# Optimization experiments

Hardware: AMD Instinct MI355X
Metric: run time of the kernel (lower is better)

## Reference

```python
import jax, jax.numpy as jnp
import numpy as np

NEG_SLOPE = 0.2  # leaky_relu_negative_slope


def setup_inputs() -> dict:
    key = jax.random.key(0)
    k = jax.random.split(key, 6)
    N = 1024          # n_nodes == nei_nodes (forced by the asserts in forward)
    IN = 256          # in_features
    OUT = 256         # out_features (nei_embedding feature dim, since linear_r = Linear(out_features, ...))
    H, F = 4, 64      # n_heads, n_hidden = out_features // n_heads
    h = jax.random.normal(k[0], (N, IN), dtype=jnp.float32)
    nei_embedding = jax.random.normal(k[1], (N, OUT), dtype=jnp.float32)
    adj_mat = jax.random.randint(k[2], (N, N), 0, 2).astype(jnp.float32)
    scale = 0.05
    w_l = jax.random.normal(k[3], (IN, H * F), dtype=jnp.float32) * scale   # linear_l.weight.T
    w_r = jax.random.normal(k[4], (OUT, H * F), dtype=jnp.float32) * scale  # linear_r.weight.T
    attn_w = jax.random.normal(k[5], (F,), dtype=jnp.float32) * scale       # attn.weight (1, F) -> (F,)
    return {"h": h, "nei_embedding": nei_embedding, "adj_mat": adj_mat,
            "w_l": w_l, "w_r": w_r, "attn_w": attn_w, "use_elu": 1}


def reference(h, nei_embedding, adj_mat, w_l, w_r, attn_w, use_elu):
    N = h.shape[0]
    M = nei_embedding.shape[0]
    F = attn_w.shape[0]
    H = w_l.shape[1] // F
    g_l = (h @ w_l).reshape(N, H, F)              # (N, H, F)
    g_r = (nei_embedding @ w_r).reshape(M, H, F)  # (M, H, F)
    # Torch does repeat/repeat_interleave then view(n, m, H, F); with the
    # assert-enforced n == m this is exactly g_sum[i, j] = g_l[j] + g_r[i].
    g_sum = g_r[:, None, :, :] + g_l[None, :, :, :]          # (N, N, H, F)
    e = jnp.einsum("nmhf,f->nmh", jax.nn.leaky_relu(g_sum, NEG_SLOPE), attn_w)
    adj_t = adj_mat.T[:, :, None]                             # (M, N, 1) -> broadcasts over heads
    e = jnp.where(adj_t == 0, -jnp.inf, e)
    exp_attention = jnp.exp(e)
    weighted = exp_attention * adj_t                          # (N, N, H)
    denom = jnp.sum(weighted, axis=1, keepdims=True)
    a = weighted / denom                                      # masked softmax over neighbors
    # dropout is identity at inference
    attn_res = jnp.einsum("ijh,jhf->ihf", a, g_r)            # (N, H, F)
    if use_elu:
        attn_res = jax.nn.elu(attn_res)
    return attn_res.reshape(N, H * F)  # is_concat=True
```

## Files before the change

kernel.cpp:

```cpp
#include <hip/hip_runtime.h>
#include <math.h>

#define NN 1024
#define KK 256
#define NH 4
#define FD 64
#define HF 256
#define RL 68
#define NG 17

typedef __attribute__((ext_vector_type(16))) float fx16;
typedef __attribute__((ext_vector_type(4)))  float fx4;

#define OFF_GR    0
#define OFF_GL2   262144
#define OFF_GR2   540672
#define OFF_CL    819200
#define OFF_CR    823296
#define OFF_DENP  827392
#define OFF_P     1089536
#define OFF_ACCP  5283840
#define OFF_DEST  13672448
#define OFF_ABSW  13672512
#define OFF_GPOS  13672576

__global__ void gatv2_prep(const float* __restrict__ aw, float* __restrict__ ws)
{
    const int f = threadIdx.x;
    const float wv = aw[f];
    const bool pos = (wv >= 0.f);
    const unsigned long long mask = __ballot(pos);
    const int npos  = __popcll(mask);
    const int npos4 = (npos + 3) & ~3;
    const unsigned long long lt = (1ull << f) - 1ull;
    const int prank = __popcll(mask & lt);
    const int nrank = __popcll(~mask & lt);
    const int dest  = pos ? prank : (npos4 + nrank);
    ((int*)(ws + OFF_DEST))[f] = dest;
    (ws + OFF_ABSW)[f] = fabsf(wv);
    if (f == 0) ((int*)(ws + OFF_GPOS))[0] = npos4 >> 2;
}

__global__ __launch_bounds__(256) void gatv2_gemm(
    const float* __restrict__ hmat, const float* __restrict__ nei,
    const float* __restrict__ w_l, const float* __restrict__ w_r,
    const float* __restrict__ aw, float* __restrict__ ws)
{
    __shared__ float sA[16*260];
    const int t   = threadIdx.x;
    const int mb  = blockIdx.x;
    const int hd  = blockIdx.y;
    const int mat = blockIdx.z;
    const float* A = mat ? nei : hmat;
    const float* W = mat ? w_r : w_l;
    float* CC = ws + (mat ? OFF_CR : OFF_CL);

    #pragma unroll
    for (int rep = 0; rep < 4; ++rep) {
        const int flat = rep*256 + t;
        const int r = flat >> 6, c = (flat & 63) << 2;
        *(float4*)&sA[r*260 + c] = *(const float4*)&A[(size_t)(mb*16 + r)*KK + c];
    }
    __syncthreads();

    const int m  = t >> 4;
    const int nq = t & 15;
    const int ng = hd*64 + (nq << 2);
    const float* Wp = W + ng;

    float4 acc = make_float4(0.f, 0.f, 0.f, 0.f);
    #pragma unroll 4
    for (int k0 = 0; k0 < KK; k0 += 4) {
        const float4 a4 = *(const float4*)&sA[m*260 + k0];
        const float4 w0 = *(const float4*)(Wp + (size_t)(k0+0)*HF);
        const float4 w1 = *(const float4*)(Wp + (size_t)(k0+1)*HF);
        const float4 w2 = *(const float4*)(Wp + (size_t)(k0+2)*HF);
        const float4 w3 = *(const float4*)(Wp + (size_t)(k0+3)*HF);
        acc.x += a4.x*w0.x; acc.y += a4.x*w0.y; acc.z += a4.x*w0.z; acc.w += a4.x*w0.w;
        acc.x += a4.y*w1.x; acc.y += a4.y*w1.y; acc.z += a4.y*w1.z; acc.w += a4.y*w1.w;
        acc.x += a4.z*w2.x; acc.y += a4.z*w2.y; acc.z += a4.z*w2.z; acc.w += a4.z*w2.w;
        acc.x += a4.w*w3.x; acc.y += a4.w*w3.y; acc.z += a4.w*w3.z; acc.w += a4.w*w3.w;
    }

    const int node = mb*16 + m;
    if (mat) *(float4*)&(ws + OFF_GR)[(size_t)node*HF + ng] = acc;

    {
        const int*   destp = (const int*)(ws + OFF_DEST);
        const int4   dv = ((const int4*)destp)[nq];
        const float4 av = ((const float4*)(ws + OFF_ABSW))[nq];
        float* g2 = ws + (mat ? OFF_GR2 : OFF_GL2) + ((size_t)node*NH + hd)*RL;
        g2[dv.x] = av.x*acc.x; g2[dv.y] = av.y*acc.y;
        g2[dv.z] = av.z*acc.z; g2[dv.w] = av.w*acc.w;
    }

    {
        const float4 w4 = ((const float4*)aw)[nq];
        float wd = w4.x*acc.x + w4.y*acc.y + w4.z*acc.z + w4.w*acc.w;
        wd += __shfl_xor(wd, 1);
        wd += __shfl_xor(wd, 2);
        wd += __shfl_xor(wd, 4);
        wd += __shfl_xor(wd, 8);
        if (nq == 0) CC[hd*NN + node] = 0.6f*wd;
    }
}

__global__ __launch_bounds__(256, 2) void gatv2_e(
    const float* __restrict__ wsro, const float* __restrict__ adj,
    float* __restrict__ P, float* __restrict__ denP)
{
    __shared__ float sgl[16*RL];
    __shared__ float scl[16];
    const float* gl2 = wsro + OFF_GL2;
    const float* gr2 = wsro + OFF_GR2;
    const float* cl  = wsro + OFF_CL;
    const float* cr  = wsro + OFF_CR;
    const int t  = threadIdx.x;
    const int jc = blockIdx.x;
    const int ib = blockIdx.y;
    const int hh = blockIdx.z;
    const int i0 = ib*512 + t;
    const int i1 = i0 + 256;
    const int j0 = jc*16;

    for (int idx = t; idx < 16*NG; idx += 256) {
        const int r = idx / NG, c = idx - r*NG;
        *(float4*)&sgl[r*RL + (c<<2)] =
            *(const float4*)&gl2[((size_t)(j0+r)*NH + hh)*RL + (c<<2)];
    }
    if (t < 16) scl[t] = cl[hh*NN + j0 + t];

    fx4 ga[NG], gb[NG];
    {
        const fx4* pa = (const fx4*)(gr2 + ((size_t)i0*NH + hh)*RL);
        const fx4* pb = (const fx4*)(gr2 + ((size_t)i1*NH + hh)*RL);
        #pragma unroll
        for (int g = 0; g < NG; ++g) { ga[g] = pa[g]; gb[g] = pb[g]; }
    }
    #pragma unroll
    for (int g = 0; g < NG; ++g) { asm volatile("" : "+v"(ga[g])); }
    #pragma unroll
    for (int g = 0; g < NG; ++g) { asm volatile("" : "+v"(gb[g])); }

    const int gpos = ((const int*)(wsro + OFF_GPOS))[0];
    float mg[NG];
    #pragma unroll
    for (int g = 0; g < NG; ++g) mg[g] = (g < gpos) ? 0.4f : -0.4f;
    #pragma unroll
    for (int g = 0; g < NG; ++g) { asm volatile("" : "+v"(mg[g])); }

    const float cr0 = cr[hh*NN + i0];
    const float cr1 = cr[hh*NN + i1];

    float den0 = 0.f, den1 = 0.f;
    __syncthreads();

    #pragma unroll 2
    for (int jj = 0; jj < 16; ++jj) {
        const int j = j0 + jj;
        const float mk0 = adj[(size_t)j*NN + i0];
        const float mk1 = adj[(size_t)j*NN + i1];
        float a0 = 0.f, a1 = 0.f;
        #pragma unroll
        for (int g = 0; g < NG; ++g) {
            const fx4 b  = *(const fx4*)&sgl[jj*RL + (g<<2)];
            const fx4 va = b + ga[g];
            const fx4 vb = b + gb[g];
            const float sa = (fabsf(va[0]) + fabsf(va[1])) + (fabsf(va[2]) + fabsf(va[3]));
            const float sb = (fabsf(vb[0]) + fabsf(vb[1])) + (fabsf(vb[2]) + fabsf(vb[3]));
            a0 = fmaf(mg[g], sa, a0);
            a1 = fmaf(mg[g], sb, a1);
        }
        const float clj = scl[jj];
        const float p0 = (mk0 != 0.f) ? __expf(cr0 + clj + a0) : 0.f;
        const float p1 = (mk1 != 0.f) ? __expf(cr1 + clj + a1) : 0.f;
        den0 += p0; den1 += p1;
        const size_t pb = ((size_t)hh*NN + j)*NN;
        P[pb + i0] = p0;
        P[pb + i1] = p1;
    }
    denP[((size_t)jc*NH + hh)*NN + i0] = den0;
    denP[((size_t)jc*NH + hh)*NN + i1] = den1;
}

#define PVFMA(G0, G1, PP)                                           \
    { _Pragma("unroll") for (int q = 0; q < 4; ++q) {               \
        acc[q].x   += (PP)*G0[q*4+0]; acc[q].y   += (PP)*G0[q*4+1]; \
        acc[q].z   += (PP)*G0[q*4+2]; acc[q].w   += (PP)*G0[q*4+3]; \
        acc[4+q].x += (PP)*G1[q*4+0]; acc[4+q].y += (PP)*G1[q*4+1]; \
        acc[4+q].z += (PP)*G1[q*4+2]; acc[4+q].w += (PP)*G1[q*4+3]; } }

__global__ __launch_bounds__(256, 4) void gatv2_pv(
    const float* __restrict__ wsro, float* __restrict__ accP)
{
    __shared__ float sT[256*36];
    const float* g_r = wsro + OFF_GR;
    const float* P   = wsro + OFF_P;
    const int t  = threadIdx.x;
    const int jc = blockIdx.x;
    const int ib = blockIdx.y;
    const int fs = blockIdx.z;
    const int hh = fs >> 1;
    const int f0 = hh*64 + (fs & 1)*32;
    const int i  = ib*256 + t;

    float4 acc[8];
    #pragma unroll
    for (int q = 0; q < 8; ++q) acc[q] = make_float4(0.f,0.f,0.f,0.f);

    const int j0 = jc*32;
    const size_t pb0 = ((size_t)hh*NN)*NN + i;

    fx16 a0, a1, b0, b1;
    {
        const float* gp = g_r + (size_t)j0*HF + f0;
        asm volatile(
            "s_load_dwordx16 %0, %2, 0x0\n\t"
            "s_load_dwordx16 %1, %2, 0x40\n\t"
            "s_waitcnt lgkmcnt(0)"
            : "=s"(a0), "=s"(a1) : "s"(gp));
    }
    float pA = P[pb0 + (size_t)j0*NN];

    for (int jj = 0; jj < 32; jj += 2) {
        const int j = j0 + jj;
        {
            const float* gp = g_r + (size_t)(j+1)*HF + f0;
            asm volatile(
                "s_load_dwordx16 %0, %2, 0x0\n\t"
                "s_load_dwordx16 %1, %2, 0x40"
                : "=s"(b0), "=s"(b1) : "s"(gp));
        }
        const float pB = P[pb0 + (size_t)(j+1)*NN];
        PVFMA(a0, a1, pA)
        asm volatile("s_waitcnt lgkmcnt(0)");
        {
            const int j2 = (jj + 2 < 32) ? (j + 2) : j0;
            const float* gp = g_r + (size_t)j2*HF + f0;
            asm volatile(
                "s_load_dwordx16 %0, %2, 0x0\n\t"
                "s_load_dwordx16 %1, %2, 0x40"
                : "=s"(a0), "=s"(a1) : "s"(gp));
            pA = P[pb0 + (size_t)j2*NN];
        }
        PVFMA(b0, b1, pB)
        asm volatile("s_waitcnt lgkmcnt(0)");
    }

    #pragma unroll
    for (int q = 0; q < 4; ++q) {
        *(float4*)&sT[t*36 + q*4] = acc[q];
        *(float4*)&sT[t*36 + 16 + q*4] = acc[4+q];
    }
    __syncthreads();
    #pragma unroll
    for (int rep = 0; rep < 8; ++rep) {
        const int idx = rep*256 + t;
        const int il = idx >> 3, fq = idx & 7;
        const float4 v = *(const float4*)&sT[il*36 + fq*4];
        *(float4*)&accP[(size_t)jc*(NN*HF) + (size_t)(ib*256 + il)*HF + f0 + fq*4] = v;
    }
}

__global__ __launch_bounds__(256) void gatv2_fin(
    const float* __restrict__ accP, const float* __restrict__ denP,
    const int* __restrict__ use_elu, float* __restrict__ out)
{
    const int idx4 = blockIdx.x*256 + threadIdx.x;
    const int i  = idx4 >> 6;
    const int hh = (idx4 >> 4) & 3;
    float4 s = make_float4(0.f,0.f,0.f,0.f);
    for (int c = 0; c < 32; ++c) {
        const float4 v = *(const float4*)&accP[(size_t)c*(NN*HF) + (size_t)idx4*4];
        s.x += v.x; s.y += v.y; s.z += v.z; s.w += v.w;
    }
    float d = 0.f;
    for (int c = 0; c < 64; ++c) d += denP[((size_t)c*NH + hh)*NN + i];
    const float rd = 1.f / d;
    float4 r = make_float4(s.x*rd, s.y*rd, s.z*rd, s.w*rd);
    if (*use_elu != 0) {
        r.x = (r.x > 0.f) ? r.x : expm1f(r.x);
        r.y = (r.y > 0.f) ? r.y : expm1f(r.y);
        r.z = (r.z > 0.f) ? r.z : expm1f(r.z);
        r.w = (r.w > 0.f) ? r.w : expm1f(r.w);
    }
    ((float4*)out)[idx4] = r;
}

extern "C" void kernel_launch(void* const* d_in, const int* in_sizes, int n_in,
                              void* d_out, int out_size, void* d_ws, size_t ws_size,
                              hipStream_t stream)
{
    const float* hmat = (const float*)d_in[0];
    const float* nei  = (const float*)d_in[1];
    const float* adj  = (const float*)d_in[2];
    const float* w_l  = (const float*)d_in[3];
    const float* w_r  = (const float*)d_in[4];
    const float* aw   = (const float*)d_in[5];
    const int*   uel  = (const int*)d_in[6];
    float* out = (float*)d_out;
    float* ws  = (float*)d_ws;

    hipMemsetAsync((void*)(ws + OFF_GL2), 0, (size_t)2*278528*sizeof(float), stream);
    hipLaunchKernelGGL(gatv2_prep, dim3(1), dim3(64), 0, stream, aw, ws);
    hipLaunchKernelGGL(gatv2_gemm, dim3(64,4,2), dim3(256), 0, stream,
                       hmat, nei, w_l, w_r, aw, ws);
    hipLaunchKernelGGL(gatv2_e, dim3(64,2,4), dim3(256), 0, stream,
                       ws, adj, ws + OFF_P, ws + OFF_DENP);
    hipLaunchKernelGGL(gatv2_pv, dim3(32,4,8), dim3(256), 0, stream,
                       ws, ws + OFF_ACCP);
    hipLaunchKernelGGL(gatv2_fin, dim3((NN*HF)/1024), dim3(256), 0, stream,
                       ws + OFF_ACCP, ws + OFF_DENP, uel, out);
}
```

Baseline: 147.2 us.

## Load g_l rows via scalar loads instead of LDS, one node per thread

The attention-score kernel stops staging the 16 g_l rows and cl values in shared memory. Each iteration now loads the wave-uniform g_l row and cl value straight into scalar registers with inline s_load_dwordx16 instructions, so the vector ALU reads them as SGPR operands. Each thread now handles one node instead of two, the grid doubles in y, and launch bounds rise to three blocks per SM for more occupancy. The cost is a full lgkmcnt wait on every j iteration, which serializes scalar memory latency, and half the reuse of each loaded g_l row.

```diff
diff --git a/kernel.cpp b/kernel.cpp
--- a/kernel.cpp
+++ b/kernel.cpp
@@ -105,12 +105,21 @@
     }
 }
 
-__global__ __launch_bounds__(256, 2) void gatv2_e(
+#define EGRP(RS, QB, q)                                             \
+    { const fx4 gq = g[(QB)+(q)];                                   \
+      const float t0 = RS[(q)*4+0] + gq[0];                         \
+      const float t1 = RS[(q)*4+1] + gq[1];                         \
+      const float t2 = RS[(q)*4+2] + gq[2];                         \
+      const float t3 = RS[(q)*4+3] + gq[3];                         \
+      a = fmaf(mg[(QB)+(q)],                                        \
+               (fabsf(t0)+fabsf(t1))+(fabsf(t2)+fabsf(t3)), a); }
+
+#define EBLK4(RS, QB) EGRP(RS, QB, 0) EGRP(RS, QB, 1) EGRP(RS, QB, 2) EGRP(RS, QB, 3)
+
+__global__ __launch_bounds__(256, 3) void gatv2_e(
     const float* __restrict__ wsro, const float* __restrict__ adj,
     float* __restrict__ P, float* __restrict__ denP)
 {
-    __shared__ float sgl[16*RL];
-    __shared__ float scl[16];
     const float* gl2 = wsro + OFF_GL2;
     const float* gr2 = wsro + OFF_GR2;
     const float* cl  = wsro + OFF_CL;
@@ -119,68 +128,56 @@
     const int jc = blockIdx.x;
     const int ib = blockIdx.y;
     const int hh = blockIdx.z;
-    const int i0 = ib*512 + t;
-    const int i1 = i0 + 256;
+    const int i  = ib*256 + t;
     const int j0 = jc*16;
 
-    for (int idx = t; idx < 16*NG; idx += 256) {
-        const int r = idx / NG, c = idx - r*NG;
-        *(float4*)&sgl[r*RL + (c<<2)] =
-            *(const float4*)&gl2[((size_t)(j0+r)*NH + hh)*RL + (c<<2)];
-    }
-    if (t < 16) scl[t] = cl[hh*NN + j0 + t];
-
-    fx4 ga[NG], gb[NG];
+    fx4 g[NG];
     {
-        const fx4* pa = (const fx4*)(gr2 + ((size_t)i0*NH + hh)*RL);
-        const fx4* pb = (const fx4*)(gr2 + ((size_t)i1*NH + hh)*RL);
+        const fx4* gp = (const fx4*)(gr2 + ((size_t)i*NH + hh)*RL);
         #pragma unroll
-        for (int g = 0; g < NG; ++g) { ga[g] = pa[g]; gb[g] = pb[g]; }
-    }
-    #pragma unroll
-    for (int g = 0; g < NG; ++g) { asm volatile("" : "+v"(ga[g])); }
-    #pragma unroll
-    for (int g = 0; g < NG; ++g) { asm volatile("" : "+v"(gb[g])); }
+        for (int q = 0; q < NG; ++q) g[q] = gp[q];
+    }
+    #pragma unroll
+    for (int q = 0; q < NG; ++q) { asm volatile("" : "+v"(g[q])); }
 
     const int gpos = ((const int*)(wsro + OFF_GPOS))[0];
     float mg[NG];
     #pragma unroll
-    for (int g = 0; g < NG; ++g) mg[g] = (g < gpos) ? 0.4f : -0.4f;
-    #pragma unroll
-    for (int g = 0; g < NG; ++g) { asm volatile("" : "+v"(mg[g])); }
-
-    const float cr0 = cr[hh*NN + i0];
-    const float cr1 = cr[hh*NN + i1];
-
-    float den0 = 0.f, den1 = 0.f;
-    __syncthreads();
-
-    #pragma unroll 2
+    for (int q = 0; q < NG; ++q) mg[q] = (q < gpos) ? 0.4f : -0.4f;
+    #pragma unroll
+    for (int q = 0; q < NG; ++q) { asm volatile("" : "+v"(mg[q])); }
+
+    const float cri = cr[hh*NN + i];
+
+    float denl = 0.f;
     for (int jj = 0; jj < 16; ++jj) {
         const int j = j0 + jj;
-        const float mk0 = adj[(size_t)j*NN + i0];
-        const float mk1 = adj[(size_t)j*NN + i1];
-        float a0 = 0.f, a1 = 0.f;
-        #pragma unroll
-        for (int g = 0; g < NG; ++g) {
-            const fx4 b  = *(const fx4*)&sgl[jj*RL + (g<<2)];
-            const fx4 va = b + ga[g];
-            const fx4 vb = b + gb[g];
-            const float sa = (fabsf(va[0]) + fabsf(va[1])) + (fabsf(va[2]) + fabsf(va[3]));
-            const float sb = (fabsf(vb[0]) + fabsf(vb[1])) + (fabsf(vb[2]) + fabsf(vb[3]));
-            a0 = fmaf(mg[g], sa, a0);
-            a1 = fmaf(mg[g], sb, a1);
+        const float mask = adj[(size_t)j*NN + i];
+
+        fx16 r0, r1, r2, r3; fx4 r4; float clv;
+        {
+            const float* rowp = gl2 + ((size_t)j*NH + hh)*RL;
+            const float* clp  = cl + hh*NN + j;
+            asm volatile(
+                "s_load_dwordx16 %0, %6, 0x0\n\t"
+                "s_load_dwordx16 %1, %6, 0x40\n\t"
+                "s_load_dwordx16 %2, %6, 0x80\n\t"
+                "s_load_dwordx16 %3, %6, 0xc0\n\t"
+                "s_load_dwordx4  %4, %6, 0x100\n\t"
+                "s_load_dword %5, %7, 0x0\n\t"
+                "s_waitcnt lgkmcnt(0)"
+                : "=s"(r0), "=s"(r1), "=s"(r2), "=s"(r3), "=s"(r4), "=s"(clv)
+                : "s"(rowp), "s"(clp));
         }
-        const float clj = scl[jj];
-        const float p0 = (mk0 != 0.f) ? __expf(cr0 + clj + a0) : 0.f;
-        const float p1 = (mk1 != 0.f) ? __expf(cr1 + clj + a1) : 0.f;
-        den0 += p0; den1 += p1;
-        const size_t pb = ((size_t)hh*NN + j)*NN;
-        P[pb + i0] = p0;
-        P[pb + i1] = p1;
-    }
-    denP[((size_t)jc*NH + hh)*NN + i0] = den0;
-    denP[((size_t)jc*NH + hh)*NN + i1] = den1;
+        float a = 0.f;
+        EBLK4(r0, 0) EBLK4(r1, 4) EBLK4(r2, 8) EBLK4(r3, 12)
+        EGRP(r4, 16, 0)
+        const float e  = cri + clv + a;
+        const float pw = (mask != 0.f) ? __expf(e) : 0.f;
+        denl += pw;
+        P[((size_t)hh*NN + j)*NN + i] = pw;
+    }
+    denP[((size_t)jc*NH + hh)*NN + i] = denl;
 }
 
 #define PVFMA(G0, G1, PP)                                           \
@@ -305,7 +302,7 @@
     hipLaunchKernelGGL(gatv2_prep, dim3(1), dim3(64), 0, stream, aw, ws);
     hipLaunchKernelGGL(gatv2_gemm, dim3(64,4,2), dim3(256), 0, stream,
                        hmat, nei, w_l, w_r, aw, ws);
-    hipLaunchKernelGGL(gatv2_e, dim3(64,2,4), dim3(256), 0, stream,
+    hipLaunchKernelGGL(gatv2_e, dim3(64,4,4), dim3(256), 0, stream,
                        ws, adj, ws + OFF_P, ws + OFF_DENP);
     hipLaunchKernelGGL(gatv2_pv, dim3(32,4,8), dim3(256), 0, stream,
                        ws, ws + OFF_ACCP);
```

New measurement: 145.0 us. Within noise of the previous version (-1.5%).
